# Optimization experiments

Hardware: AMD Instinct MI355X
Metric: run time of the kernel (lower is better)

Reference implementation:

```python
import jax, jax.numpy as jnp
import numpy as np

N_HEADS = 8
HEAD_DIM = 32
GROUPS = 32
EPS = 1e-5


def setup_inputs() -> dict:
    key = jax.random.key(0)
    ks = jax.random.split(key, 3)
    b, c, h, w = 8, 256, 32, 32
    x = jax.random.normal(ks[0], (b, c, h, w), dtype=jnp.float32)
    norm_w = jnp.ones((c,), dtype=jnp.float32)
    norm_b = jnp.zeros((c,), dtype=jnp.float32)
    qkv_w = jax.random.normal(ks[1], (3 * c, c), dtype=jnp.float32) * (c ** -0.5)
    qkv_b = jnp.zeros((3 * c,), dtype=jnp.float32)
    out_w = jax.random.normal(ks[2], (c, c), dtype=jnp.float32) * (c ** -0.5)
    out_b = jnp.zeros((c,), dtype=jnp.float32)
    return {"x": x, "norm_w": norm_w, "norm_b": norm_b,
            "qkv_w": qkv_w, "qkv_b": qkv_b, "out_w": out_w, "out_b": out_b}


def _group_norm(x, weight, bias):
    b, c, h, w = x.shape
    xr = x.reshape(b, GROUPS, -1)  # [b, 32, (c//32)*h*w]
    mu = xr.mean(axis=-1, keepdims=True)
    var = xr.var(axis=-1, keepdims=True)
    xn = ((xr - mu) * jax.lax.rsqrt(var + EPS)).reshape(b, c, h, w)
    return xn * weight[:, None, None] + bias[:, None, None]


def _conv1x1(x, w, b):
    # 1x1 conv == channel matmul
    return jnp.einsum('oc,bchw->bohw', w, x) + b[None, :, None, None]


def reference(x, norm_w, norm_b, qkv_w, qkv_b, out_w, out_b):
    b, c, h, w = x.shape
    hw = h * w
    scale = HEAD_DIM ** (-0.5)
    qkv = _conv1x1(_group_norm(x, norm_w, norm_b), qkv_w, qkv_b)  # [b, 3c, h, w]
    q, k, v = jnp.split(qkv, 3, axis=1)
    # torch reshape(b, n_heads, c//n_heads, h*w) is a raw row-major reshape
    q = q.reshape(b, N_HEADS, HEAD_DIM, hw) * scale
    k = k.reshape(b, N_HEADS, HEAD_DIM, hw)
    v = v.reshape(b, N_HEADS, HEAD_DIM, hw)
    sim = jnp.einsum('bhdi,bhdj->bhij', q, k)  # [b, heads, hw, hw]
    sim = sim - jax.lax.stop_gradient(sim.max(axis=-1, keepdims=True))
    attn = jax.nn.softmax(sim, axis=-1)
    out = jnp.einsum('bhij,bhdj->bhid', attn, v)  # [b, heads, hw, head_dim]
    # faithful to the original: raw reshape (b, heads, hw, head_dim) -> (b, c, h, w)
    out = out.reshape(b, c, h, w)
    return _conv1x1(out, out_w, out_b) + x
```

## Files before the change

### kernel.cpp

```cpp
#include <hip/hip_runtime.h>
#include <hip/hip_bf16.h>

#define NB 8
#define NC 256
#define NHW 1024

typedef unsigned short u16;
typedef unsigned int u32;
using f16x8  = __attribute__((ext_vector_type(8))) _Float16;
using f32x16 = __attribute__((ext_vector_type(16))) float;
using u32x4  = __attribute__((ext_vector_type(4))) unsigned int;
using u16x8  = __attribute__((ext_vector_type(8))) unsigned short;

static __device__ inline u16 f2h(float f) {
    _Float16 h = (_Float16)f;
    return __builtin_bit_cast(u16, h);
}
static __device__ inline float h2f(u16 u) {
    return (float)__builtin_bit_cast(_Float16, u);
}
static __device__ inline unsigned pk2(float a, float b) {
    auto r = __builtin_amdgcn_cvt_pkrtz(a, b);
    return __builtin_bit_cast(unsigned, r);
}
static __device__ inline void gload16(const void* g, void* l) {
    __builtin_amdgcn_global_load_lds(
        (const __attribute__((address_space(1))) void*)g,
        (__attribute__((address_space(3))) void*)l, 16, 0, 0);
}
static __device__ inline float vmax16(const f32x16& v) {
    float m0 = fmaxf(fmaxf(v[0], v[1]), fmaxf(v[2], v[3]));
    float m1 = fmaxf(fmaxf(v[4], v[5]), fmaxf(v[6], v[7]));
    float m2 = fmaxf(fmaxf(v[8], v[9]), fmaxf(v[10], v[11]));
    float m3 = fmaxf(fmaxf(v[12], v[13]), fmaxf(v[14], v[15]));
    return fmaxf(fmaxf(m0, m1), fmaxf(m2, m3));
}
static __device__ inline float vsum16(const f32x16& v) {
    float s0 = (v[0] + v[1]) + (v[2] + v[3]);
    float s1 = (v[4] + v[5]) + (v[6] + v[7]);
    float s2 = (v[8] + v[9]) + (v[10] + v[11]);
    float s3 = (v[12] + v[13]) + (v[14] + v[15]);
    return (s0 + s1) + (s2 + s3);
}
template<int B>
static __device__ inline f16x8 packP(const f32x16& p, const int h) {
    unsigned u0 = pk2(p[B + 0], p[B + 1]);
    unsigned u1 = pk2(p[B + 2], p[B + 3]);
    unsigned u2 = pk2(p[B + 4], p[B + 5]);
    unsigned u3 = pk2(p[B + 6], p[B + 7]);
    unsigned pu0 = __shfl_xor(u0, 32);
    unsigned pu1 = __shfl_xor(u1, 32);
    unsigned pu2 = __shfl_xor(u2, 32);
    unsigned pu3 = __shfl_xor(u3, 32);
    u32x4 w;
    w[0] = h ? pu2 : u0;
    w[1] = h ? pu3 : u1;
    w[2] = h ? u2 : pu0;
    w[3] = h ? u3 : pu1;
    return __builtin_bit_cast(f16x8, w);
}

#define QSCALE 0.25505412f

__global__ __launch_bounds__(256) void prep_kernel(
    const float* __restrict__ x, const float* __restrict__ qkv_w,
    const float* __restrict__ out_w, float2* __restrict__ stats,
    u16* __restrict__ Wq, u16* __restrict__ Wo)
{
    __shared__ float rs[4][2];
    const int bid = blockIdx.x, t = threadIdx.x;
    if (bid < 256) {
        const int g = bid & 31, b = bid >> 5;
        const size_t base = ((size_t)b * NC + g * 8) * NHW;
        const float4* xi = (const float4*)(x + base);
        float sum = 0.f, sq = 0.f;
#pragma unroll
        for (int i = 0; i < 8; ++i) {
            float4 v = xi[t + i * 256];
            sum += v.x + v.y + v.z + v.w;
            sq += v.x * v.x + v.y * v.y + v.z * v.z + v.w * v.w;
        }
        const int lane = t & 63, wv = t >> 6;
#pragma unroll
        for (int o = 32; o > 0; o >>= 1) {
            sum += __shfl_down(sum, o, 64);
            sq += __shfl_down(sq, o, 64);
        }
        if (lane == 0) { rs[wv][0] = sum; rs[wv][1] = sq; }
        __syncthreads();
        if (t == 0) {
            float S = rs[0][0] + rs[1][0] + rs[2][0] + rs[3][0];
            float Q = rs[0][1] + rs[1][1] + rs[2][1] + rs[3][1];
            float mu = S * (1.f / 8192.f);
            float var = Q * (1.f / 8192.f) - mu * mu;
            stats[b * 32 + g] = make_float2(mu, rsqrtf(var + 1e-5f));
        }
    } else {
        const int f4 = (bid - 256) * 256 + t;
        float4 v;
        u16* dhp;
        int e;
        if (f4 < 49152) {
            e = f4 * 4;
            v = *(const float4*)&qkv_w[e];
            if ((e >> 8) < 256) {
                v.x *= QSCALE; v.y *= QSCALE; v.z *= QSCALE; v.w *= QSCALE;
            }
            dhp = Wq;
        } else {
            e = (f4 - 49152) * 4;
            v = *(const float4*)&out_w[e];
            dhp = Wo;
        }
        ushort4 hh;
        hh.x = f2h(v.x); hh.y = f2h(v.y); hh.z = f2h(v.z); hh.w = f2h(v.w);
        *(ushort4*)&dhp[e] = hh;
    }
}

__global__ __launch_bounds__(256) void qkv_gemm_kernel(
    const u16* __restrict__ W, const float* __restrict__ x,
    const float2* __restrict__ stats,
    const float* __restrict__ gw, const float* __restrict__ gb,
    const float* __restrict__ bias,
    u16* __restrict__ qT, u16* __restrict__ kT, u16* __restrict__ vN)
{
    __shared__ __align__(16) u16 sB[2][2048];
    const int b = blockIdx.z;
    const int m0 = blockIdx.y * 128, n0 = blockIdx.x * 64;
    const int t = threadIdx.x, w = t >> 6, lane = t & 63;
    const int l31 = lane & 31, h = lane >> 5;
    const int msub = m0 + w * 32;

    const u16* War = W + (size_t)(msub + l31) * 256 + h * 8;

    const float bscale = (msub < 256) ? QSCALE : 1.0f;
    f32x16 acc[2];
#pragma unroll
    for (int r = 0; r < 16; ++r) {
        const int crow = (r & 3) + 8 * (r >> 2) + 4 * h;
        const float bv = bias[msub + crow] * bscale;
        acc[0][r] = bv; acc[1][r] = bv;
    }

    const int sn = t & 63;
    const int sw = w;
    const float* xs = x + (size_t)b * 256 * 1024 + (size_t)(sw * 8) * 1024 + n0 + sn;
    float vreg[8];
    const int woff = sn * 32 + ((sw ^ ((sn >> 1) & 3)) * 8);

#define LOADX(kcn) { _Pragma("unroll") for (int j = 0; j < 8; ++j) \
        vreg[j] = xs[(size_t)((kcn) * 32 + j) * 1024]; }
#define STAGE(kcn, buf) { \
        const int cb = (kcn) * 32 + sw * 8; \
        const float2 st = stats[b * 32 + (cb >> 3)]; \
        u32x4 pkv; \
        _Pragma("unroll") for (int jp = 0; jp < 4; ++jp) { \
            const float sc0 = gw[cb + jp * 2] * st.y; \
            const float of0 = gb[cb + jp * 2] - st.x * sc0; \
            const float sc1 = gw[cb + jp * 2 + 1] * st.y; \
            const float of1 = gb[cb + jp * 2 + 1] - st.x * sc1; \
            pkv[jp] = pk2(vreg[jp * 2] * sc0 + of0, vreg[jp * 2 + 1] * sc1 + of1); } \
        *(u32x4*)&sB[buf][woff] = pkv; }

    LOADX(0);
    STAGE(0, 0);
    __syncthreads();
    int cur = 0;
    for (int kc = 0; kc < 8; ++kc) {
        if (kc < 7) LOADX(kc + 1);
#pragma unroll
        for (int k16 = 0; k16 < 2; ++k16) {
            const f16x8 ah = *(const f16x8*)(War + kc * 32 + k16 * 16);
#pragma unroll
            for (int ns = 0; ns < 2; ++ns) {
                const int row = ns * 32 + l31;
                const int gi = ((k16 * 2 + h) ^ ((row >> 1) & 3)) * 8;
                const f16x8 bh = *(const f16x8*)&sB[cur][row * 32 + gi];
                acc[ns] = __builtin_amdgcn_mfma_f32_32x32x16_f16(ah, bh, acc[ns], 0, 0, 0);
            }
        }
        if (kc < 7) STAGE(kc + 1, cur ^ 1);
        __syncthreads();
        cur ^= 1;
    }
#undef LOADX
#undef STAGE

    const int type = msub >> 8;
    const int head = (msub >> 5) & 7;
    const int bh_ = b * 8 + head;
    if (type < 2) {
        u16* dst = type ? kT : qT;
#pragma unroll
        for (int ns = 0; ns < 2; ++ns) {
            const int n = n0 + ns * 32 + l31;
            u16* p = dst + ((size_t)bh_ * 1024 + n) * 32;
#pragma unroll
            for (int rp = 0; rp < 8; ++rp) {
                const int r = rp * 2;
                const int d = (r & 3) + 8 * (r >> 2) + 4 * h;
                *(unsigned*)&p[d] = (unsigned)f2h(acc[ns][r]) | ((unsigned)f2h(acc[ns][r + 1]) << 16);
            }
        }
    } else {
#pragma unroll
        for (int ns = 0; ns < 2; ++ns) {
            const int n = n0 + ns * 32 + l31;
#pragma unroll
            for (int r = 0; r < 16; ++r) {
                const int d = (r & 3) + 8 * (r >> 2) + 4 * h;
                vN[((size_t)bh_ * 32 + d) * 1024 + n] = f2h(acc[ns][r]);
            }
        }
    }
}

__global__ __launch_bounds__(256) void attn_mfma_kernel(
    const u16* __restrict__ qT, const u16* __restrict__ kT,
    const u16* __restrict__ vN, u16* __restrict__ ao)
{
    __shared__ __align__(16) u16 Ks[2][2048];
    __shared__ __align__(16) u16 Vs[2][2048];
    const int bid = blockIdx.x;
    const int itile = bid >> 6, bh = bid & 63;
    const int b = bh >> 3, head = bh & 7;
    const int t = threadIdx.x;
    const int lane = t & 63;
    const int w = t >> 6;
    const int l31 = lane & 31;
    const int h = lane >> 5;
    const int ibase = itile * 128 + w * 32;

    const u16* qrow = qT + ((size_t)bh * 1024 + ibase + l31) * 32;
    const f16x8 qf0 = *(const f16x8*)(qrow + h * 8);
    const f16x8 qf1 = *(const f16x8*)(qrow + 16 + h * 8);

    f32x16 out = {};
    float m = -1e30f, lsum = 0.f;

    const u16* ksrc = kT + ((size_t)bh * 1024 + (t >> 2)) * 32 + ((t & 3) ^ ((t >> 2) & 3)) * 8;
    const u16* vsrc = vN + ((size_t)bh * 32 + (t >> 3)) * 1024 + ((t & 7) ^ ((t >> 3) & 7)) * 8;
    const int wseg = w * 512;

    gload16(ksrc, &Ks[0][wseg]);
    gload16(vsrc, &Vs[0][wseg]);
    __syncthreads();
    int cur = 0;
    for (int T = 0; T < 16; ++T) {
        if (T < 15) {
            gload16(ksrc + (size_t)(T + 1) * 2048, &Ks[cur ^ 1][wseg]);
            gload16(vsrc + (T + 1) * 64, &Vs[cur ^ 1][wseg]);
        }
        const int gk0 = (h ^ (l31 & 3)) * 8;
        const int gk1 = ((2 + h) ^ (l31 & 3)) * 8;
        const f16x8 kf00 = *(const f16x8*)&Ks[cur][l31 * 32 + gk0];
        const f16x8 kf01 = *(const f16x8*)&Ks[cur][l31 * 32 + gk1];
        const f16x8 kf10 = *(const f16x8*)&Ks[cur][(32 + l31) * 32 + gk0];
        const f16x8 kf11 = *(const f16x8*)&Ks[cur][(32 + l31) * 32 + gk1];
        f32x16 sA = {}, sB = {};
        sA = __builtin_amdgcn_mfma_f32_32x32x16_f16(kf00, qf0, sA, 0, 0, 0);
        sA = __builtin_amdgcn_mfma_f32_32x32x16_f16(kf01, qf1, sA, 0, 0, 0);
        sB = __builtin_amdgcn_mfma_f32_32x32x16_f16(kf10, qf0, sB, 0, 0, 0);
        sB = __builtin_amdgcn_mfma_f32_32x32x16_f16(kf11, qf1, sB, 0, 0, 0);

        float mt = fmaxf(vmax16(sA), vmax16(sB));
        mt = fmaxf(mt, __shfl_xor(mt, 32));
        if (!__all(mt <= m + 8.f)) {
            const float mn = fmaxf(m, mt);
            const float cor = exp2f(m - mn);
            m = mn;
            lsum *= cor;
#pragma unroll
            for (int r = 0; r < 16; ++r) {
                const int src = (r & 3) + 8 * (r >> 2) + 4 * h;
                out[r] *= __shfl(cor, src);
            }
        }
#pragma unroll
        for (int r = 0; r < 16; ++r) {
            sA[r] = exp2f(sA[r] - m);
            sB[r] = exp2f(sB[r] - m);
        }
        float ps = vsum16(sA) + vsum16(sB);
        ps += __shfl_xor(ps, 32);
        lsum += ps;

        const f16x8 pf0 = packP<0>(sA, h);
        const f16x8 pf1 = packP<8>(sA, h);
        const f16x8 pf2 = packP<0>(sB, h);
        const f16x8 pf3 = packP<8>(sB, h);
        const int vx = l31 & 7;
        const f16x8 vf0 = *(const f16x8*)&Vs[cur][l31 * 64 + ((h    ) ^ vx) * 8];
        const f16x8 vf1 = *(const f16x8*)&Vs[cur][l31 * 64 + ((2 + h) ^ vx) * 8];
        const f16x8 vf2 = *(const f16x8*)&Vs[cur][l31 * 64 + ((4 + h) ^ vx) * 8];
        const f16x8 vf3 = *(const f16x8*)&Vs[cur][l31 * 64 + ((6 + h) ^ vx) * 8];
        out = __builtin_amdgcn_mfma_f32_32x32x16_f16(pf0, vf0, out, 0, 0, 0);
        out = __builtin_amdgcn_mfma_f32_32x32x16_f16(pf1, vf1, out, 0, 0, 0);
        out = __builtin_amdgcn_mfma_f32_32x32x16_f16(pf2, vf2, out, 0, 0, 0);
        out = __builtin_amdgcn_mfma_f32_32x32x16_f16(pf3, vf3, out, 0, 0, 0);
        __syncthreads();
        cur ^= 1;
    }

    const float linv = 1.f / lsum;
    const int cOut = b * 256 + head * 32 + itile * 4 + w;
    u16* og = ao + (size_t)cOut * 1024 + l31;
#pragma unroll
    for (int r = 0; r < 16; ++r) {
        const int crow = (r & 3) + 8 * (r >> 2) + 4 * h;
        const float sc = __shfl(linv, crow);
        og[crow * 32] = f2h(out[r] * sc);
    }
}

__global__ __launch_bounds__(256) void out_gemm_kernel(
    const u16* __restrict__ W, const u16* __restrict__ ao,
    const float* __restrict__ bias,
    const float* __restrict__ res, float* __restrict__ Y)
{
    __shared__ __align__(16) u16 sB[2][2048];
    const int b = blockIdx.z;
    const int m0 = blockIdx.y * 64, n0 = blockIdx.x * 64;
    const int t = threadIdx.x, w = t >> 6, lane = t & 63;
    const int l31 = lane & 31, h = lane >> 5;
    const int wm = w >> 1, wn = w & 1;
    const int msub = m0 + wm * 32;

    const u16* War = W + (size_t)(msub + l31) * 256 + h * 8;

    f32x16 acc;
#pragma unroll
    for (int r = 0; r < 16; ++r) {
        const int crow = (r & 3) + 8 * (r >> 2) + 4 * h;
        acc[r] = bias[msub + crow];
    }

    const int kL = t >> 3, pb = (t & 7) * 8;
    const u16* asrc = ao + ((size_t)b * 256 + kL) * 1024 + n0 + pb;
    u16x8 regs;

#define LOADC(kc) { regs = *(const u16x8*)(asrc + (size_t)(kc) * 32 * 1024); }
#define WRITEC(buf) { _Pragma("unroll") for (int e = 0; e < 8; ++e) { \
        const int n = pb + e; \
        const int idx = n * 32 + ((kL >> 3) ^ (n & 3)) * 8 + (kL & 7); \
        sB[buf][idx] = regs[e]; } }

    LOADC(0); WRITEC(0);
    __syncthreads();
    int cur = 0;
    for (int kc = 0; kc < 8; ++kc) {
        if (kc < 7) LOADC(kc + 1);
#pragma unroll
        for (int k16 = 0; k16 < 2; ++k16) {
            const f16x8 ah = *(const f16x8*)(War + kc * 32 + k16 * 16);
            const int gi = ((k16 * 2 + h) ^ (l31 & 3)) * 8;
            const int row = wn * 32 + l31;
            const f16x8 bh = *(const f16x8*)&sB[cur][row * 32 + gi];
            acc = __builtin_amdgcn_mfma_f32_32x32x16_f16(ah, bh, acc, 0, 0, 0);
        }
        if (kc < 7) WRITEC(cur ^ 1);
        __syncthreads();
        cur ^= 1;
    }
    const int n = n0 + wn * 32 + l31;
#pragma unroll
    for (int r = 0; r < 16; ++r) {
        const int mm = msub + (r & 3) + 8 * (r >> 2) + 4 * h;
        const size_t idx = ((size_t)b * 256 + mm) * 1024 + n;
        Y[idx] = acc[r] + res[idx];
    }
#undef LOADC
#undef WRITEC
}

extern "C" void kernel_launch(void* const* d_in, const int* in_sizes, int n_in,
                              void* d_out, int out_size, void* d_ws, size_t ws_size,
                              hipStream_t stream) {
    const float* x      = (const float*)d_in[0];
    const float* norm_w = (const float*)d_in[1];
    const float* norm_b = (const float*)d_in[2];
    const float* qkv_w  = (const float*)d_in[3];
    const float* qkv_b  = (const float*)d_in[4];
    const float* out_w  = (const float*)d_in[5];
    const float* out_b  = (const float*)d_in[6];
    float* out = (float*)d_out;

    char* p = (char*)d_ws;
    float2* stats = (float2*)p;  p += 4096;
    u16* Wq  = (u16*)p;  p += 393216 * 2;
    u16* Wo  = (u16*)p;  p += 131072 * 2;
    u16* qT  = (u16*)p;  p += 4u * 1024 * 1024;
    u16* kT  = (u16*)p;  p += 4u * 1024 * 1024;
    u16* vN  = (u16*)p;  p += 4u * 1024 * 1024;
    u16* ao  = (u16*)p;  p += 4u * 1024 * 1024;

    prep_kernel<<<512, 256, 0, stream>>>(x, qkv_w, out_w, stats, Wq, Wo);
    qkv_gemm_kernel<<<dim3(16, 6, NB), 256, 0, stream>>>(Wq, x, stats, norm_w, norm_b, qkv_b, qT, kT, vN);
    attn_mfma_kernel<<<512, 256, 0, stream>>>(qT, kT, vN, ao);
    out_gemm_kernel<<<dim3(16, 4, NB), 256, 0, stream>>>(Wo, ao, out_b, x, out);
}
```

Measured before the change: 67.66 us.

## Load K/V fragments directly from global into registers, drop LDS staging

The attention kernel stops staging K and V tiles in double-buffered shared memory via global_load_lds with barriers. Instead each lane loads its MFMA operand fragments straight from global memory into registers, software-pipelined one tile ahead with two register sets. This removes LDS traffic and the per-tile __syncthreads. In exchange, the four waves of a block now each load the same K/V data from global/L2 instead of sharing it, which increases cache traffic and register pressure.

Result: no change. 68.37 us (+1.1%).

```diff
diff --git a/kernel.cpp b/kernel.cpp
--- a/kernel.cpp
+++ b/kernel.cpp
@@ -22,11 +22,6 @@
 static __device__ inline unsigned pk2(float a, float b) {
     auto r = __builtin_amdgcn_cvt_pkrtz(a, b);
     return __builtin_bit_cast(unsigned, r);
-}
-static __device__ inline void gload16(const void* g, void* l) {
-    __builtin_amdgcn_global_load_lds(
-        (const __attribute__((address_space(1))) void*)g,
-        (__attribute__((address_space(3))) void*)l, 16, 0, 0);
 }
 static __device__ inline float vmax16(const f32x16& v) {
     float m0 = fmaxf(fmaxf(v[0], v[1]), fmaxf(v[2], v[3]));
@@ -220,8 +215,6 @@
     const u16* __restrict__ qT, const u16* __restrict__ kT,
     const u16* __restrict__ vN, u16* __restrict__ ao)
 {
-    __shared__ __align__(16) u16 Ks[2][2048];
-    __shared__ __align__(16) u16 Vs[2][2048];
     const int bid = blockIdx.x;
     const int itile = bid >> 6, bh = bid & 63;
     const int b = bh >> 3, head = bh & 7;
@@ -239,69 +232,69 @@
     f32x16 out = {};
     float m = -1e30f, lsum = 0.f;
 
-    const u16* ksrc = kT + ((size_t)bh * 1024 + (t >> 2)) * 32 + ((t & 3) ^ ((t >> 2) & 3)) * 8;
-    const u16* vsrc = vN + ((size_t)bh * 32 + (t >> 3)) * 1024 + ((t & 7) ^ ((t >> 3) & 7)) * 8;
-    const int wseg = w * 512;
-
-    gload16(ksrc, &Ks[0][wseg]);
-    gload16(vsrc, &Vs[0][wseg]);
-    __syncthreads();
-    int cur = 0;
-    for (int T = 0; T < 16; ++T) {
-        if (T < 15) {
-            gload16(ksrc + (size_t)(T + 1) * 2048, &Ks[cur ^ 1][wseg]);
-            gload16(vsrc + (T + 1) * 64, &Vs[cur ^ 1][wseg]);
-        }
-        const int gk0 = (h ^ (l31 & 3)) * 8;
-        const int gk1 = ((2 + h) ^ (l31 & 3)) * 8;
-        const f16x8 kf00 = *(const f16x8*)&Ks[cur][l31 * 32 + gk0];
-        const f16x8 kf01 = *(const f16x8*)&Ks[cur][l31 * 32 + gk1];
-        const f16x8 kf10 = *(const f16x8*)&Ks[cur][(32 + l31) * 32 + gk0];
-        const f16x8 kf11 = *(const f16x8*)&Ks[cur][(32 + l31) * 32 + gk1];
-        f32x16 sA = {}, sB = {};
-        sA = __builtin_amdgcn_mfma_f32_32x32x16_f16(kf00, qf0, sA, 0, 0, 0);
-        sA = __builtin_amdgcn_mfma_f32_32x32x16_f16(kf01, qf1, sA, 0, 0, 0);
-        sB = __builtin_amdgcn_mfma_f32_32x32x16_f16(kf10, qf0, sB, 0, 0, 0);
-        sB = __builtin_amdgcn_mfma_f32_32x32x16_f16(kf11, qf1, sB, 0, 0, 0);
-
-        float mt = fmaxf(vmax16(sA), vmax16(sB));
-        mt = fmaxf(mt, __shfl_xor(mt, 32));
-        if (!__all(mt <= m + 8.f)) {
-            const float mn = fmaxf(m, mt);
-            const float cor = exp2f(m - mn);
-            m = mn;
-            lsum *= cor;
-#pragma unroll
-            for (int r = 0; r < 16; ++r) {
-                const int src = (r & 3) + 8 * (r >> 2) + 4 * h;
-                out[r] *= __shfl(cor, src);
-            }
-        }
-#pragma unroll
-        for (int r = 0; r < 16; ++r) {
-            sA[r] = exp2f(sA[r] - m);
-            sB[r] = exp2f(sB[r] - m);
-        }
-        float ps = vsum16(sA) + vsum16(sB);
-        ps += __shfl_xor(ps, 32);
-        lsum += ps;
-
-        const f16x8 pf0 = packP<0>(sA, h);
-        const f16x8 pf1 = packP<8>(sA, h);
-        const f16x8 pf2 = packP<0>(sB, h);
-        const f16x8 pf3 = packP<8>(sB, h);
-        const int vx = l31 & 7;
-        const f16x8 vf0 = *(const f16x8*)&Vs[cur][l31 * 64 + ((h    ) ^ vx) * 8];
-        const f16x8 vf1 = *(const f16x8*)&Vs[cur][l31 * 64 + ((2 + h) ^ vx) * 8];
-        const f16x8 vf2 = *(const f16x8*)&Vs[cur][l31 * 64 + ((4 + h) ^ vx) * 8];
-        const f16x8 vf3 = *(const f16x8*)&Vs[cur][l31 * 64 + ((6 + h) ^ vx) * 8];
-        out = __builtin_amdgcn_mfma_f32_32x32x16_f16(pf0, vf0, out, 0, 0, 0);
-        out = __builtin_amdgcn_mfma_f32_32x32x16_f16(pf1, vf1, out, 0, 0, 0);
-        out = __builtin_amdgcn_mfma_f32_32x32x16_f16(pf2, vf2, out, 0, 0, 0);
-        out = __builtin_amdgcn_mfma_f32_32x32x16_f16(pf3, vf3, out, 0, 0, 0);
-        __syncthreads();
-        cur ^= 1;
-    }
+    const u16* kb = kT + (size_t)bh * 32768 + (size_t)l31 * 32 + h * 8;
+    const u16* vb = vN + (size_t)bh * 32768 + (size_t)l31 * 1024 + h * 8;
+
+    f16x8 ck0, ck1, ck2, ck3, cv0, cv1, cv2, cv3;
+    f16x8 nk0, nk1, nk2, nk3, nv0, nv1, nv2, nv3;
+
+#define LOADT(T, K0, K1, K2, K3, V0, V1, V2, V3) { \
+    const u16* kp = kb + (T) * 2048; \
+    K0 = *(const f16x8*)(kp); \
+    K1 = *(const f16x8*)(kp + 16); \
+    K2 = *(const f16x8*)(kp + 1024); \
+    K3 = *(const f16x8*)(kp + 1024 + 16); \
+    const u16* vp = vb + (T) * 64; \
+    V0 = *(const f16x8*)(vp); \
+    V1 = *(const f16x8*)(vp + 16); \
+    V2 = *(const f16x8*)(vp + 32); \
+    V3 = *(const f16x8*)(vp + 48); }
+
+#define STEP(K0, K1, K2, K3, V0, V1, V2, V3) { \
+    f32x16 sA = {}, sB = {}; \
+    sA = __builtin_amdgcn_mfma_f32_32x32x16_f16(K0, qf0, sA, 0, 0, 0); \
+    sA = __builtin_amdgcn_mfma_f32_32x32x16_f16(K1, qf1, sA, 0, 0, 0); \
+    sB = __builtin_amdgcn_mfma_f32_32x32x16_f16(K2, qf0, sB, 0, 0, 0); \
+    sB = __builtin_amdgcn_mfma_f32_32x32x16_f16(K3, qf1, sB, 0, 0, 0); \
+    float mt = fmaxf(vmax16(sA), vmax16(sB)); \
+    mt = fmaxf(mt, __shfl_xor(mt, 32)); \
+    if (!__all(mt <= m + 8.f)) { \
+        const float mn = fmaxf(m, mt); \
+        const float cor = exp2f(m - mn); \
+        m = mn; \
+        lsum *= cor; \
+        _Pragma("unroll") for (int r = 0; r < 16; ++r) { \
+            const int src = (r & 3) + 8 * (r >> 2) + 4 * h; \
+            out[r] *= __shfl(cor, src); \
+        } \
+    } \
+    _Pragma("unroll") for (int r = 0; r < 16; ++r) { \
+        sA[r] = exp2f(sA[r] - m); \
+        sB[r] = exp2f(sB[r] - m); \
+    } \
+    float ps = vsum16(sA) + vsum16(sB); \
+    ps += __shfl_xor(ps, 32); \
+    lsum += ps; \
+    const f16x8 pf0 = packP<0>(sA, h); \
+    const f16x8 pf1 = packP<8>(sA, h); \
+    const f16x8 pf2 = packP<0>(sB, h); \
+    const f16x8 pf3 = packP<8>(sB, h); \
+    out = __builtin_amdgcn_mfma_f32_32x32x16_f16(pf0, V0, out, 0, 0, 0); \
+    out = __builtin_amdgcn_mfma_f32_32x32x16_f16(pf1, V1, out, 0, 0, 0); \
+    out = __builtin_amdgcn_mfma_f32_32x32x16_f16(pf2, V2, out, 0, 0, 0); \
+    out = __builtin_amdgcn_mfma_f32_32x32x16_f16(pf3, V3, out, 0, 0, 0); }
+
+    LOADT(0, ck0, ck1, ck2, ck3, cv0, cv1, cv2, cv3);
+    for (int T2 = 0; T2 < 8; ++T2) {
+        LOADT(2 * T2 + 1, nk0, nk1, nk2, nk3, nv0, nv1, nv2, nv3);
+        STEP(ck0, ck1, ck2, ck3, cv0, cv1, cv2, cv3);
+        if (T2 < 7) {
+            LOADT(2 * T2 + 2, ck0, ck1, ck2, ck3, cv0, cv1, cv2, cv3);
+        }
+        STEP(nk0, nk1, nk2, nk3, nv0, nv1, nv2, nv3);
+    }
+#undef LOADT
+#undef STEP
 
     const float linv = 1.f / lsum;
     const int cOut = b * 256 + head * 32 + itile * 4 + w;
```
